# Kernel tuning notes

Measured on AMD Instinct MI355X. Metric: run time of the kernel, lower is better.

Reference implementation:

```python
import jax, jax.numpy as jnp
import numpy as np

# FTDEA(e_hidden=300, r_hidden=100, t_hidden=100)
N_NODES = 50000
N_EDGES = 250000
N_EDGES_ALL = 500000
N_REL = 300
EH, RH, TH = 300, 100, 100


def _seg_softmax(logits, seg, num):
    # torch_geometric.utils.softmax: segment-wise stable softmax
    m = jax.ops.segment_max(logits, seg, num_segments=num)
    e = jnp.exp(logits - m[seg])
    s = jax.ops.segment_sum(e, seg, num_segments=num)
    return e / s[seg]


def _gcn(x, j, i, n):
    deg = jax.ops.segment_sum(jnp.ones(i.shape[0], x.dtype), i, num_segments=n)
    dinv = jnp.where(deg > 0, 1.0 / jnp.sqrt(jnp.maximum(deg, 1.0)), 0.0)
    norm = dinv[j] * dinv[i]
    return jax.nn.relu(jax.ops.segment_sum(norm[:, None] * x[j], i, num_segments=n))


def setup_inputs():
    key = jax.random.key(0)
    ks = jax.random.split(key, 32)
    f32 = jnp.float32

    def w(k, shape):
        return jax.random.normal(k, shape, f32) / np.float32(np.sqrt(shape[0]))

    inp = {
        "x": jax.random.normal(ks[0], (N_NODES, EH), f32),
        "edge_index": jax.random.randint(ks[1], (2, N_EDGES), 0, N_NODES),
        "rel": jax.random.randint(ks[2], (N_EDGES,), 0, N_REL),
        "edge_index_all": jax.random.randint(ks[3], (2, N_EDGES_ALL), 0, N_NODES),
        "rel_size": jnp.arange(N_EDGES),
        "hw1_w": w(ks[4], (EH, EH)), "hw1_b": jnp.zeros((EH,), f32),
        "hw2_w": w(ks[5], (EH, EH)), "hw2_b": jnp.zeros((EH,), f32),
        "tc1_w": w(ks[6], (EH, TH)), "tc1_b": jnp.zeros((TH,), f32),
        "sr1_w": w(ks[7], (2 * TH, RH)), "sr1_b": jnp.zeros((RH,), f32),
        "a1_w": w(ks[8], (RH,)), "a5_w": w(ks[9], (RH,)),
        "wr_w": w(ks[10], (RH + 2 * TH, EH)), "wr_b": jnp.zeros((EH,), f32),
        "wr1_w": w(ks[11], (RH + 2 * TH, EH)), "wr1_b": jnp.zeros((EH,), f32),
        "wr2_w": w(ks[12], (RH + 2 * TH, EH)), "wr2_b": jnp.zeros((EH,), f32),
        "ah_w": w(ks[13], (EH,)), "ah1_w": w(ks[14], (EH,)), "at_w": w(ks[15], (EH,)),
        "ar1_w": w(ks[16], (EH,)), "ar2_w": w(ks[17], (EH,)), "ar3_w": w(ks[18], (EH,)),
        "ai_w": w(ks[19], (EH,)), "aj_w": w(ks[20], (EH,)),
        "fc_w": w(ks[21], (2 * EH,)), "fc_b": jnp.zeros((1,), f32),
    }
    return inp


def _forward(x, hw1_w, hw1_b, hw2_w, hw2_b, tc1_w, tc1_b, sr1_w, sr1_b, a1_w, a5_w,
             wr_w, wr_b, wr1_w, wr1_b, wr2_w, wr2_b, ah_w, ah1_w, at_w,
             ar1_w, ar2_w, ar3_w, ai_w, aj_w, fc_w, fc_b,
             edge_index, rel, edge_index_all, rel_size):
    N = x.shape[0]
    E = rel.shape[0]
    h, t = edge_index[0], edge_index[1]
    j, i = edge_index_all[0], edge_index_all[1]
    lrelu = jax.nn.leaky_relu  # slope 0.01 == F.leaky_relu default

    def highway(x1, x2, wg, bg):
        gate = jax.nn.sigmoid(x1 @ wg + bg)
        return gate * x2 + (1.0 - gate) * x1

    x = highway(x, _gcn(x, j, i, N), hw1_w, hw1_b)
    x = highway(x, _gcn(x, j, i, N), hw2_w, hw2_b)

    # --- GATt_to_R. NB: FTDEA overwrites gat_e_to_r output with zeros, so
    # x_res1 input is all-zeros and GAT_E_to_R is mathematically dead code.
    # Also r_in_t1 aliases r_in_t in the torch code, so the in-place per-relation
    # mean loop rewrites BOTH -> r_in_t1 = per-relation mean features.
    s = x @ tc1_w + tc1_b                                    # [N, t]
    cnt = jnp.maximum(jax.ops.segment_sum(jnp.ones(E, x.dtype), rel, num_segments=N_REL), 1.0)[:, None]
    mh = jax.ops.segment_sum(s[h], rel, num_segments=N_REL) / cnt
    mt = jax.ops.segment_sum(s[t], rel, num_segments=N_REL) / cnt
    r_in_t1 = jnp.concatenate([mh, mt], axis=1)[rel]         # [E, 2t]
    x_res2 = r_in_t1 @ sr1_w + sr1_b                         # [E, r]
    x_res1 = jnp.zeros((E, RH), x.dtype)                     # zeroed GAT_E_to_R output
    e1 = x_res2 @ a1_w + x_res1 @ a5_w                       # [E]
    alpha = _seg_softmax(lrelu(e1), rel, N_REL)
    x_type = jax.ops.segment_sum(alpha[:, None] * x_res2[rel_size], rel, num_segments=N_REL)  # spmm
    r_f = jnp.concatenate([x_res1 + x_type[rel], r_in_t1], axis=1)   # [E, r+2t]

    # --- GATr_to_e: three attention rounds (head, tail, head) ---
    def r2e(x_e, wr, br, a_node, a_rel, idx):
        e_r = r_f @ wr + br                                  # [E, e]
        logits = x_e[idx] @ a_node + e_r @ a_rel             # [E]
        a = _seg_softmax(lrelu(logits), idx, N)
        agg = jax.nn.relu(jax.ops.segment_sum(a[:, None] * e_r[rel_size], idx, num_segments=N))
        return x_e + agg

    x = r2e(x, wr_w, wr_b, ah_w, ar1_w, h)
    x = r2e(x, wr1_w, wr1_b, at_w, ar2_w, t)
    x = r2e(x, wr2_w, wr2_b, ah1_w, ar3_w, h)

    # --- GAT_act over edge_index_all ---
    logits = (x @ ai_w)[i] + (x @ aj_w)[j]
    a = _seg_softmax(lrelu(logits), i, N)
    g = jax.nn.relu(jax.ops.segment_sum(a[:, None] * x[j], i, num_segments=N))

    return jnp.concatenate([x, g], axis=1) @ fc_w + fc_b[0]  # [N]


def reference(x, edge_index, rel, edge_index_all, rel_size, hw1_w, hw1_b, hw2_w, hw2_b,
              tc1_w, tc1_b, sr1_w, sr1_b, a1_w, a5_w, wr_w, wr_b, wr1_w, wr1_b,
              wr2_w, wr2_b, ah_w, ah1_w, at_w, ar1_w, ar2_w, ar3_w, ai_w, aj_w, fc_w, fc_b):
    return _forward(x, hw1_w, hw1_b, hw2_w, hw2_b, tc1_w, tc1_b, sr1_w, sr1_b, a1_w, a5_w,
                    wr_w, wr_b, wr1_w, wr1_b, wr2_w, wr2_b, ah_w, ah1_w, at_w,
                    ar1_w, ar2_w, ar3_w, ai_w, aj_w, fc_w, fc_b,
                    edge_index, rel, edge_index_all, rel_size)
```

## Files before the change

kernel.cpp:

```cpp
#include <hip/hip_runtime.h>
#include <hip/hip_bf16.h>

typedef __hip_bfloat16 bf16;
typedef __attribute__((ext_vector_type(8))) short bf16x8_t;
typedef __attribute__((ext_vector_type(8))) unsigned short u16x8;
typedef __attribute__((ext_vector_type(4))) float f32x4_t;

__device__ __forceinline__ float b2f(bf16 v){ return __bfloat162float(v); }
__device__ __forceinline__ bf16 f2b(float v){ return __float2bfloat16(v); }
__device__ __forceinline__ short tobits(float v){ bf16 b = f2b(v); return *(short*)&b; }
__device__ __forceinline__ float us2f(ushort u){ return __uint_as_float(((unsigned)u)<<16); }
__device__ __forceinline__ ushort f2us(float v){ bf16 b = f2b(v); return *(ushort*)&b; }

#define NN 50000
#define NN128 50048
#define NE 250000
#define NEA 500000
#define NR 300
#define EHD 300
#define THD 100
#define RHD 100
#define XP 320
#define ERP 320
#define RCH 8
#define NBN 98
#define NBR 75

__device__ __forceinline__ int clampi(int v, int n){ return ((unsigned)v < (unsigned)n) ? v : 0; }

__device__ __forceinline__ int rdl_i(int v, int l){ return __builtin_amdgcn_readlane(v, l); }
__device__ __forceinline__ float rdl_f(float v, int l){ return __int_as_float(__builtin_amdgcn_readlane(__float_as_int(v), l)); }

typedef const __attribute__((address_space(1))) unsigned int* gas1_t;
typedef __attribute__((address_space(3))) unsigned int* las3_t;
__device__ __forceinline__ void glds16(const void* g, void* l){
    __builtin_amdgcn_global_load_lds((gas1_t)g, (las3_t)l, 16, 0, 0);
}

__device__ __forceinline__ float dpp_sum(float x){
    int v;
    v = __builtin_amdgcn_update_dpp(0, __float_as_int(x), 0x111, 0xf, 0xf, true); x += __int_as_float(v);
    v = __builtin_amdgcn_update_dpp(0, __float_as_int(x), 0x112, 0xf, 0xf, true); x += __int_as_float(v);
    v = __builtin_amdgcn_update_dpp(0, __float_as_int(x), 0x114, 0xf, 0xf, true); x += __int_as_float(v);
    v = __builtin_amdgcn_update_dpp(0, __float_as_int(x), 0x118, 0xf, 0xf, true); x += __int_as_float(v);
    v = __builtin_amdgcn_update_dpp(0, __float_as_int(x), 0x142, 0xf, 0xf, true); x += __int_as_float(v);
    v = __builtin_amdgcn_update_dpp(0, __float_as_int(x), 0x143, 0xf, 0xf, true); x += __int_as_float(v);
    return __int_as_float(__builtin_amdgcn_readlane(__float_as_int(x), 63));
}
__device__ __forceinline__ float dpp_max(float x){
    int v;
    v = __builtin_amdgcn_update_dpp(__float_as_int(x), __float_as_int(x), 0x111, 0xf, 0xf, false); x = fmaxf(x, __int_as_float(v));
    v = __builtin_amdgcn_update_dpp(__float_as_int(x), __float_as_int(x), 0x112, 0xf, 0xf, false); x = fmaxf(x, __int_as_float(v));
    v = __builtin_amdgcn_update_dpp(__float_as_int(x), __float_as_int(x), 0x114, 0xf, 0xf, false); x = fmaxf(x, __int_as_float(v));
    v = __builtin_amdgcn_update_dpp(__float_as_int(x), __float_as_int(x), 0x118, 0xf, 0xf, false); x = fmaxf(x, __int_as_float(v));
    v = __builtin_amdgcn_update_dpp(__float_as_int(x), __float_as_int(x), 0x142, 0xf, 0xf, false); x = fmaxf(x, __int_as_float(v));
    v = __builtin_amdgcn_update_dpp(__float_as_int(x), __float_as_int(x), 0x143, 0xf, 0xf, false); x = fmaxf(x, __int_as_float(v));
    return __int_as_float(__builtin_amdgcn_readlane(__float_as_int(x), 63));
}

__global__ void k_prep(const float* __restrict__ xin, ushort* __restrict__ xFu,
                       const float* __restrict__ hw1w, const float* __restrict__ hw2w,
                       const float* __restrict__ tc1w,
                       short* __restrict__ Wt1, short* __restrict__ Wt2, short* __restrict__ Wtc,
                       const float* __restrict__ ahw, const float* __restrict__ atw,
                       const float* __restrict__ ah1w, const float* __restrict__ ajw,
                       const float* __restrict__ aiw, const float* __restrict__ fcw,
                       float* __restrict__ apad, int* __restrict__ bcnt){
    int i = blockIdx.x*256 + threadIdx.x;
    if(i < 512) bcnt[i] = 0;
    const int NC = NN*40;
    const int S1 = NC + 320*320;
    const int S2 = S1 + 320*320;
    const int S3 = S2 + 128*320;
    const int S4 = S3 + 7*XP;
    if(i < NC){
        int nrow = i/40, c8 = i - nrow*40, c = c8*8;
        ushort o[8];
        if(c + 8 <= EHD){
            const float4* src = (const float4*)(xin + (size_t)nrow*EHD + c);
            float4 v0 = src[0], v1 = src[1];
            o[0]=f2us(v0.x); o[1]=f2us(v0.y); o[2]=f2us(v0.z); o[3]=f2us(v0.w);
            o[4]=f2us(v1.x); o[5]=f2us(v1.y); o[6]=f2us(v1.z); o[7]=f2us(v1.w);
        } else {
            #pragma unroll
            for(int k=0;k<8;k++){
                int cc = c + k;
                o[k] = (cc < EHD) ? f2us(xin[(size_t)nrow*EHD + cc]) : (ushort)0;
            }
        }
        u16x8 w;
        #pragma unroll
        for(int k=0;k<8;k++) w[k] = o[k];
        *(u16x8*)(xFu + (size_t)nrow*XP + c) = w;
    } else if(i < S1){
        int ii = i - NC; int n = ii/320, k = ii - n*320;
        Wt1[ii] = (n < EHD && k < EHD) ? tobits(hw1w[(size_t)k*EHD + n]) : (short)0;
    } else if(i < S2){
        int ii = i - S1; int n = ii/320, k = ii - n*320;
        Wt2[ii] = (n < EHD && k < EHD) ? tobits(hw2w[(size_t)k*EHD + n]) : (short)0;
    } else if(i < S3){
        int ii = i - S2; int n = ii/320, k = ii - n*320;
        Wtc[ii] = (n < THD && k < EHD) ? tobits(tc1w[(size_t)k*THD + n]) : (short)0;
    } else if(i < S4){
        int ii = i - S3; int v = ii/XP, c = ii - v*XP;
        float val = 0.f;
        if(c < EHD){
            const float* src = (v==0)?ahw:(v==1)?atw:(v==2)?ah1w:(v==3)?ajw:(v==4)?aiw:
                               (v==5)? fcw : (fcw + EHD);
            val = src[c];
        }
        apad[ii] = val;
    }
}

__global__ __launch_bounds__(256) void k_bincnt(const int* __restrict__ ji, const int* __restrict__ ht,
                         const int* __restrict__ rel, int* __restrict__ bcnt){
    int s = blockIdx.y;
    int n_s = (s == 0) ? NEA : NE;
    int base_e = blockIdx.x*2048;
    if(base_e >= n_s) return;
    int shift = (s < 3) ? 9 : 2;
    int tid = threadIdx.x;
    __shared__ int h[128];
    if(tid < 128) h[tid] = 0;
    __syncthreads();
    #pragma unroll
    for(int u=0;u<8;u++){
        int e = base_e + u*256 + tid;
        if(e < n_s){
            int key;
            if(s == 0) key = clampi(ji[NEA + e], NN);
            else if(s == 1) key = clampi(ht[e], NN);
            else if(s == 2) key = clampi(ht[NE + e], NN);
            else key = clampi(rel[e], NR);
            atomicAdd(&h[key >> shift], 1);
        }
    }
    __syncthreads();
    if(tid < 128 && h[tid] > 0) atomicAdd(&bcnt[s*128 + tid], h[tid]);
}

__global__ void k_bscan(const int* __restrict__ bcnt, int* __restrict__ gbase, int* __restrict__ gcur){
    __shared__ int lds[512];
    int tid = threadIdx.x;
    int v = bcnt[tid];
    lds[tid] = v; __syncthreads();
    for(int st=1; st<128; st<<=1){
        int add = ((tid & 127) >= st) ? lds[tid-st] : 0;
        __syncthreads();
        lds[tid] += add;
        __syncthreads();
    }
    int s = tid >> 7, b = tid & 127;
    int excl = lds[tid] - v;
    gbase[s*129 + b] = excl;
    gcur[s*128 + b] = excl;
    if(b == 127) gbase[s*129 + 128] = lds[tid];
}

__global__ __launch_bounds__(256) void k_bin(const int* __restrict__ ji, const int* __restrict__ ht,
                      const int* __restrict__ rel, int* __restrict__ gcur,
                      int2* __restrict__ t0, int2* __restrict__ t1,
                      int2* __restrict__ t2, int2* __restrict__ t3){
    int s = blockIdx.y;
    int n_s = (s == 0) ? NEA : NE;
    int base_e = blockIdx.x*2048;
    if(base_e >= n_s) return;
    int shift = (s < 3) ? 9 : 2;
    int tid = threadIdx.x;
    __shared__ int cnt[128], lof[128], base[128];
    __shared__ int2 buf[2048];
    if(tid < 128) cnt[tid] = 0;
    __syncthreads();
    int kk[8], pp[8], bb[8], ss[8];
    #pragma unroll
    for(int u=0;u<8;u++){
        int e = base_e + u*256 + tid;
        bb[u] = -1;
        if(e < n_s){
            int key, pay;
            if(s == 0){ key = clampi(ji[NEA + e], NN); pay = clampi(ji[e], NN); }
            else if(s == 1){ key = clampi(ht[e], NN); pay = clampi(rel[e], NR); }
            else if(s == 2){ key = clampi(ht[NE + e], NN); pay = clampi(rel[e], NR); }
            else { key = clampi(rel[e], NR); pay = e; }
            int b = key >> shift;
            kk[u] = key; pp[u] = pay; bb[u] = b;
            ss[u] = atomicAdd(&cnt[b], 1);
        }
    }
    __syncthreads();
    if(tid == 0){
        int run = 0;
        for(int b=0;b<128;b++){ lof[b] = run; run += cnt[b]; }
    }
    __syncthreads();
    #pragma unroll
    for(int u=0;u<8;u++){
        if(bb[u] >= 0){
            int pos = lof[bb[u]] + ss[u];
            buf[pos] = make_int2(kk[u], pp[u]);
        }
    }
    __syncthreads();
    if(tid < 128 && cnt[tid] > 0) base[tid] = atomicAdd(&gcur[s*128 + tid], cnt[tid]);
    __syncthreads();
    int2* tmp = (s==0) ? t0 : (s==1) ? t1 : (s==2) ? t2 : t3;
    int total = lof[127] + cnt[127];
    for(int idx=tid; idx<total; idx+=256){
        int2 kp = buf[idx];
        int b = kp.x >> shift;
        tmp[base[b] + (idx - lof[b])] = kp;
    }
}

__global__ __launch_bounds__(256) void k_place(const int* __restrict__ gbase,
                        const int2* __restrict__ t0, const int2* __restrict__ t1,
                        const int2* __restrict__ t2, const int2* __restrict__ t3,
                        int* __restrict__ off_all, int* __restrict__ off_h,
                        int* __restrict__ off_t, int* __restrict__ off_r,
                        int* __restrict__ adj_all, int* __restrict__ adj_h,
                        int* __restrict__ adj_t, int* __restrict__ adj_r,
                        float* __restrict__ dinv){
    int s = blockIdx.y, b = blockIdx.x;
    int NB = (s < 3) ? NBN : NBR;
    if(b >= NB) return;
    int W = (s < 3) ? 512 : 4;
    int len = (s < 3) ? NN : NR;
    const int2* tmp = (s==0) ? t0 : (s==1) ? t1 : (s==2) ? t2 : t3;
    int* off = (s==0) ? off_all : (s==1) ? off_h : (s==2) ? off_t : off_r;
    int* adj = (s==0) ? adj_all : (s==1) ? adj_h : (s==2) ? adj_t : adj_r;
    int node0 = b*W;
    int node1 = node0 + W; if(node1 > len) node1 = len;
    int nloc = node1 - node0;
    int wstart = gbase[s*129 + b], wend = gbase[s*129 + b + 1];
    __shared__ int hist[512];
    __shared__ int cur[512];
    __shared__ int sb[256];
    int tid = threadIdx.x;
    for(int k=tid; k<nloc; k+=256) hist[k] = 0;
    __syncthreads();
    for(int idx = wstart + tid; idx < wend; idx += 256){
        int local = tmp[idx].x - node0;
        if((unsigned)local < (unsigned)nloc) atomicAdd(&hist[local], 1);
    }
    __syncthreads();
    int v0 = (2*tid   < nloc) ? hist[2*tid]   : 0;
    int v1 = (2*tid+1 < nloc) ? hist[2*tid+1] : 0;
    int ps = v0 + v1;
    sb[tid] = ps; __syncthreads();
    for(int st=1; st<256; st<<=1){
        int add = (tid >= st) ? sb[tid-st] : 0;
        __syncthreads();
        sb[tid] += add;
        __syncthreads();
    }
    int excl = sb[tid] - ps;
    if(2*tid < nloc){
        int o = wstart + excl;
        off[node0 + 2*tid] = o;
        cur[2*tid] = o;
        if(s == 0) dinv[node0 + 2*tid] = v0 > 0 ? rsqrtf((float)v0) : 0.f;
    }
    if(2*tid+1 < nloc){
        int o = wstart + excl + v0;
        off[node0 + 2*tid+1] = o;
        cur[2*tid+1] = o;
        if(s == 0) dinv[node0 + 2*tid+1] = v1 > 0 ? rsqrtf((float)v1) : 0.f;
    }
    if(b == NB-1 && tid == 0) off[len] = gbase[s*129 + 128];
    __syncthreads();
    for(int idx = wstart + tid; idx < wend; idx += 256){
        int2 kp = tmp[idx];
        int local = kp.x - node0;
        if((unsigned)local < (unsigned)nloc){
            int slot = atomicAdd(&cur[local], 1);
            adj[slot] = kp.y;
        }
    }
}

__global__ void k_gcn(const bf16* __restrict__ xs, bf16* __restrict__ xd,
                      const int* __restrict__ off, const int* __restrict__ adjj,
                      const float* __restrict__ dinv){
    int wid = threadIdx.x >> 6, lane = threadIdx.x & 63;
    int n = blockIdx.x*4 + wid;
    if(n >= NN) return;
    float di = dinv[n];
    int s0 = off[n], s1 = off[n+1], cnt = s1 - s0;
    bool act = lane < 40;
    float c0=0,c1=0,c2=0,c3=0,c4=0,c5=0,c6=0,c7=0;
    if(cnt > 0 && cnt <= 64){
        int jl = (lane < cnt) ? clampi(adjj[s0+lane], NN) : 0;
        float dl = (lane < cnt) ? dinv[jl] : 0.f;
        int it = 0;
        for(; it+4 <= cnt; it += 4){
            int j0=rdl_i(jl,it), j1=rdl_i(jl,it+1), j2=rdl_i(jl,it+2), j3=rdl_i(jl,it+3);
            float n0=di*rdl_f(dl,it), n1=di*rdl_f(dl,it+1), n2=di*rdl_f(dl,it+2), n3=di*rdl_f(dl,it+3);
            if(act){
                u16x8 v0 = ((const u16x8*)(xs + (size_t)j0*XP))[lane];
                u16x8 v1 = ((const u16x8*)(xs + (size_t)j1*XP))[lane];
                u16x8 v2 = ((const u16x8*)(xs + (size_t)j2*XP))[lane];
                u16x8 v3 = ((const u16x8*)(xs + (size_t)j3*XP))[lane];
                c0 += n0*us2f(v0[0])+n1*us2f(v1[0])+n2*us2f(v2[0])+n3*us2f(v3[0]);
                c1 += n0*us2f(v0[1])+n1*us2f(v1[1])+n2*us2f(v2[1])+n3*us2f(v3[1]);
                c2 += n0*us2f(v0[2])+n1*us2f(v1[2])+n2*us2f(v2[2])+n3*us2f(v3[2]);
                c3 += n0*us2f(v0[3])+n1*us2f(v1[3])+n2*us2f(v2[3])+n3*us2f(v3[3]);
                c4 += n0*us2f(v0[4])+n1*us2f(v1[4])+n2*us2f(v2[4])+n3*us2f(v3[4]);
                c5 += n0*us2f(v0[5])+n1*us2f(v1[5])+n2*us2f(v2[5])+n3*us2f(v3[5]);
                c6 += n0*us2f(v0[6])+n1*us2f(v1[6])+n2*us2f(v2[6])+n3*us2f(v3[6]);
                c7 += n0*us2f(v0[7])+n1*us2f(v1[7])+n2*us2f(v2[7])+n3*us2f(v3[7]);
            }
        }
        for(; it < cnt; it++){
            int j0 = rdl_i(jl, it);
            float n0 = di*rdl_f(dl, it);
            if(act){
                u16x8 v0 = ((const u16x8*)(xs + (size_t)j0*XP))[lane];
                c0 += n0*us2f(v0[0]); c1 += n0*us2f(v0[1]); c2 += n0*us2f(v0[2]); c3 += n0*us2f(v0[3]);
                c4 += n0*us2f(v0[4]); c5 += n0*us2f(v0[5]); c6 += n0*us2f(v0[6]); c7 += n0*us2f(v0[7]);
            }
        }
    } else if(cnt > 64){
        for(int it=s0; it<s1; it++){
            int j = clampi(adjj[it], NN);
            float nr = di * dinv[j];
            if(act){
                u16x8 v0 = ((const u16x8*)(xs + (size_t)j*XP))[lane];
                c0 += nr*us2f(v0[0]); c1 += nr*us2f(v0[1]); c2 += nr*us2f(v0[2]); c3 += nr*us2f(v0[3]);
                c4 += nr*us2f(v0[4]); c5 += nr*us2f(v0[5]); c6 += nr*us2f(v0[6]); c7 += nr*us2f(v0[7]);
            }
        }
    }
    if(act){
        u16x8 w;
        w[0]=f2us(fmaxf(c0,0.f)); w[1]=f2us(fmaxf(c1,0.f)); w[2]=f2us(fmaxf(c2,0.f)); w[3]=f2us(fmaxf(c3,0.f));
        w[4]=f2us(fmaxf(c4,0.f)); w[5]=f2us(fmaxf(c5,0.f)); w[6]=f2us(fmaxf(c6,0.f)); w[7]=f2us(fmaxf(c7,0.f));
        ((u16x8*)(xd + (size_t)n*XP))[lane] = w;
    }
}

template<int MODE>
__global__ __launch_bounds__(256) void k_gemm_mfma(const bf16* __restrict__ X,
                       const short* __restrict__ Wt, const float* __restrict__ bias,
                       bf16* __restrict__ out, const bf16* __restrict__ Xprev,
                       int M, int K, int Ncols, int ldOut){
    __shared__ short As[64*32];
    __shared__ short Bs[64*32];
    int tid = threadIdx.x;
    int bm = blockIdx.x*64, bn = blockIdx.y*64;
    int wid = tid>>6, lane = tid&63;
    int wm = (wid&1)*32, wn = (wid>>1)*32;
    int lm = lane&15, lq = lane>>4;
    f32x4_t acc00={0,0,0,0}, acc01={0,0,0,0}, acc10={0,0,0,0}, acc11={0,0,0,0};
    int srow = tid>>2, ssl = tid&3;
    int ssl_sw = ssl ^ ((srow>>1)&3);
    short* ldsA = As + (size_t)(wid*64)*8;
    short* ldsB = Bs + (size_t)(wid*64)*8;
    const bf16*  gA = X  + (size_t)(bm + srow)*K + ssl_sw*8;
    const short* gB = Wt + (size_t)(bn + srow)*K + ssl_sw*8;
    for(int k0=0; k0<K; k0+=32){
        glds16(gA + k0, ldsA);
        glds16(gB + k0, ldsB);
        __syncthreads();
        int ra0 = wm + lm, ra1 = wm + 16 + lm;
        int rb0 = wn + lm, rb1 = wn + 16 + lm;
        bf16x8_t a0 = *(const bf16x8_t*)(As + ra0*32 + ((lq ^ ((ra0>>1)&3))*8));
        bf16x8_t a1 = *(const bf16x8_t*)(As + ra1*32 + ((lq ^ ((ra1>>1)&3))*8));
        bf16x8_t b0 = *(const bf16x8_t*)(Bs + rb0*32 + ((lq ^ ((rb0>>1)&3))*8));
        bf16x8_t b1 = *(const bf16x8_t*)(Bs + rb1*32 + ((lq ^ ((rb1>>1)&3))*8));
        acc00 = __builtin_amdgcn_mfma_f32_16x16x32_bf16(a0, b0, acc00, 0, 0, 0);
        acc01 = __builtin_amdgcn_mfma_f32_16x16x32_bf16(a0, b1, acc01, 0, 0, 0);
        acc10 = __builtin_amdgcn_mfma_f32_16x16x32_bf16(a1, b0, acc10, 0, 0, 0);
        acc11 = __builtin_amdgcn_mfma_f32_16x16x32_bf16(a1, b1, acc11, 0, 0, 0);
        __syncthreads();
    }
    #pragma unroll
    for(int tm=0;tm<2;tm++){
        #pragma unroll
        for(int tn=0;tn<2;tn++){
            f32x4_t a = tm==0 ? (tn==0 ? acc00 : acc01) : (tn==0 ? acc10 : acc11);
            int gn = bn + wn + tn*16 + lm;
            if(gn >= Ncols) continue;
            float bi = bias[gn];
            #pragma unroll
            for(int r=0;r<4;r++){
                int gm = bm + wm + tm*16 + lq*4 + r;
                if(gm >= M) continue;
                float t = a[r] + bi;
                size_t p = (size_t)gm*ldOut + gn;
                if(MODE == 0){
                    out[p] = f2b(t);
                } else {
                    float g = __builtin_amdgcn_rcpf(1.f + __expf(-t));
                    out[p] = f2b(g*b2f(out[p]) + (1.f - g)*b2f(Xprev[p]));
                }
            }
        }
    }
}

__global__ void k_relsum2(const bf16* __restrict__ s, const int* __restrict__ ht,
                          const int* __restrict__ off_r, const int* __restrict__ adj_r,
                          float* __restrict__ RFpart){
    int r = blockIdx.x, c = blockIdx.y, d = threadIdx.x;
    if(d >= THD) return;
    int s0 = off_r[r], s1 = off_r[r+1];
    int cnt = s1 - s0;
    float ah = 0.f, at2 = 0.f;
    if(cnt > 0){
        int per = (cnt + RCH - 1)/RCH;
        int lo = s0 + c*per, hi = lo + per; if(hi > s1) hi = s1;
        for(int it=lo; it<hi; it++){
            int e = clampi(adj_r[it], NE);
            int hh = clampi(ht[e], NN), tt = clampi(ht[NE + e], NN);
            ah  += b2f(s[(size_t)hh*THD + d]);
            at2 += b2f(s[(size_t)tt*THD + d]);
        }
    }
    size_t base = (size_t)(r*RCH + c)*2*THD;
    RFpart[base + d] = ah;
    RFpart[base + THD + d] = at2;
}

__global__ void k_relfin(const float* __restrict__ sr1w, const float* __restrict__ sr1b,
                         const int* __restrict__ off_r, const float* __restrict__ RFpart,
                         float* __restrict__ RF){
    int r = blockIdx.x, d = threadIdx.x;
    int cnt = off_r[r+1] - off_r[r];
    float inv = 1.f/(float)(cnt > 1 ? cnt : 1);
    if(d < THD){
        float a = 0.f, b = 0.f;
        #pragma unroll
        for(int c=0;c<RCH;c++){
            size_t base = (size_t)(r*RCH + c)*2*THD;
            a += RFpart[base + d];
            b += RFpart[base + THD + d];
        }
        RF[(size_t)r*EHD + THD   + d] = a*inv;
        RF[(size_t)r*EHD + 2*THD + d] = b*inv;
    }
    __syncthreads();
    if(d < RHD){
        float v = 0.f;
        if(cnt > 0){
            v = sr1b[d];
            for(int k2=0; k2<2*THD; k2++) v += RF[(size_t)r*EHD + THD + k2] * sr1w[k2*RHD + d];
        }
        RF[(size_t)r*EHD + d] = v;
    }
}

__global__ void k_reler(const float* __restrict__ RF,
                        const float* w0, const float* b0, const float* w1, const float* b1,
                        const float* w2, const float* b2,
                        const float* ar1, const float* ar2, const float* ar3,
                        float* __restrict__ ER, float* __restrict__ cvec){
    int r = blockIdx.x, kk = blockIdx.y;
    const float* w = kk==0 ? w0 : (kk==1 ? w1 : w2);
    const float* b = kk==0 ? b0 : (kk==1 ? b1 : b2);
    const float* a = kk==0 ? ar1 : (kk==1 ? ar2 : ar3);
    int tid = threadIdx.x;
    __shared__ float rfs[EHD];
    for(int d=tid; d<EHD; d+=256) rfs[d] = RF[(size_t)r*EHD + d];
    __syncthreads();
    float pd = 0.f;
    for(int o = tid; o < ERP; o += 256){
        float v = 0.f;
        if(o < EHD){
            v = b[o];
            for(int d=0; d<EHD; d++) v += rfs[d] * w[(size_t)d*EHD + o];
            pd += v * a[o];
        }
        ER[((size_t)kk*NR + r)*ERP + o] = v;
    }
    __shared__ float red[4];
    pd = dpp_sum(pd);
    if((tid & 63) == 0) red[tid>>6] = pd;
    __syncthreads();
    if(tid == 0) cvec[kk*NR + r] = red[0]+red[1]+red[2]+red[3];
}

__device__ __forceinline__ void r2e_round(float* xv, bool act, int lane, int s0, int s1,
        int rl, float cval,
        const int* __restrict__ adjrel, const float* __restrict__ ERk,
        const float* __restrict__ ck, const float* __restrict__ an){
    float p = 0.f;
    if(act){
        const float4* a4 = (const float4*)an;
        float4 a0 = a4[2*lane], a1 = a4[2*lane+1];
        p = xv[0]*a0.x + xv[1]*a0.y + xv[2]*a0.z + xv[3]*a0.w
          + xv[4]*a1.x + xv[5]*a1.y + xv[6]*a1.z + xv[7]*a1.w;
    }
    p = dpp_sum(p);
    int cnt = s1 - s0;
    if(cnt <= 0) return;
    float c0=0,c1=0,c2=0,c3=0,c4=0,c5=0,c6=0,c7=0;
    if(cnt <= 64){
        float lg = p + cval;
        lg = lg > 0 ? lg : 0.01f*lg;
        float mx = dpp_max((lane < cnt) ? lg : -1e30f);
        float ex = (lane < cnt) ? __expf(lg - mx) : 0.f;
        float al = ex * __builtin_amdgcn_rcpf(dpp_sum(ex));
        int it = 0;
        for(; it+2 <= cnt; it += 2){
            int r0i = rdl_i(rl, it), r1i = rdl_i(rl, it+1);
            float q0 = rdl_f(al, it), q1 = rdl_f(al, it+1);
            if(act){
                const float4* e0p = (const float4*)(ERk + (size_t)r0i*ERP);
                const float4* e1p = (const float4*)(ERk + (size_t)r1i*ERP);
                float4 e0 = e0p[2*lane], e1 = e1p[2*lane];
                float4 f0 = e0p[2*lane+1], f1 = e1p[2*lane+1];
                c0 += q0*e0.x + q1*e1.x; c1 += q0*e0.y + q1*e1.y;
                c2 += q0*e0.z + q1*e1.z; c3 += q0*e0.w + q1*e1.w;
                c4 += q0*f0.x + q1*f1.x; c5 += q0*f0.y + q1*f1.y;
                c6 += q0*f0.z + q1*f1.z; c7 += q0*f0.w + q1*f1.w;
            }
        }
        if(it < cnt){
            int r0i = rdl_i(rl, it);
            float q0 = rdl_f(al, it);
            if(act){
                const float4* e0p = (const float4*)(ERk + (size_t)r0i*ERP);
                float4 e0 = e0p[2*lane], f0 = e0p[2*lane+1];
                c0 += q0*e0.x; c1 += q0*e0.y; c2 += q0*e0.z; c3 += q0*e0.w;
                c4 += q0*f0.x; c5 += q0*f0.y; c6 += q0*f0.z; c7 += q0*f0.w;
            }
        }
    } else {
        float mx = -1e30f;
        for(int it=s0; it<s1; it++){
            float lg = p + ck[clampi(adjrel[it], NR)];
            lg = lg > 0 ? lg : 0.01f*lg;
            mx = fmaxf(mx, lg);
        }
        float ssum = 0.f;
        for(int it=s0; it<s1; it++){
            float lg = p + ck[clampi(adjrel[it], NR)];
            lg = lg > 0 ? lg : 0.01f*lg;
            ssum += __expf(lg - mx);
        }
        float rinv = __builtin_amdgcn_rcpf(ssum);
        for(int it=s0; it<s1; it++){
            int r = clampi(adjrel[it], NR);
            float lg = p + ck[r];
            lg = lg > 0 ? lg : 0.01f*lg;
            float aw = __expf(lg - mx)*rinv;
            if(act){
                const float4* er4 = (const float4*)(ERk + (size_t)r*ERP);
                float4 e0 = er4[2*lane], f0 = er4[2*lane+1];
                c0 += aw*e0.x; c1 += aw*e0.y; c2 += aw*e0.z; c3 += aw*e0.w;
                c4 += aw*f0.x; c5 += aw*f0.y; c6 += aw*f0.z; c7 += aw*f0.w;
            }
        }
    }
    xv[0] += fmaxf(c0,0.f); xv[1] += fmaxf(c1,0.f); xv[2] += fmaxf(c2,0.f); xv[3] += fmaxf(c3,0.f);
    xv[4] += fmaxf(c4,0.f); xv[5] += fmaxf(c5,0.f); xv[6] += fmaxf(c6,0.f); xv[7] += fmaxf(c7,0.f);
}

__global__ void k_r2e3(bf16* __restrict__ x,
                       const int* __restrict__ off_h, const int* __restrict__ adj_h,
                       const int* __restrict__ off_t, const int* __restrict__ adj_t,
                       const float* __restrict__ ER, const float* __restrict__ cvec,
                       const float* __restrict__ apad, float* __restrict__ ajv){
    int wid = threadIdx.x >> 6, lane = threadIdx.x & 63;
    int n = blockIdx.x*4 + wid;
    if(n >= NN) return;
    bool act = lane < 40;
    u16x8* xr = (u16x8*)(x + (size_t)n*XP);
    float xv[8];
    if(act){
        u16x8 v = xr[lane];
        #pragma unroll
        for(int k=0;k<8;k++) xv[k] = us2f(v[k]);
    } else {
        #pragma unroll
        for(int k=0;k<8;k++) xv[k] = 0.f;
    }
    int h0 = off_h[n], h1 = off_h[n+1];
    int t0_ = off_t[n], t1_ = off_t[n+1];
    int hcnt = h1 - h0, tcnt = t1_ - t0_;
    int rlh = (hcnt > 0 && hcnt <= 64 && lane < hcnt) ? clampi(adj_h[h0+lane], NR) : 0;
    int rlt = (tcnt > 0 && tcnt <= 64 && lane < tcnt) ? clampi(adj_t[t0_+lane], NR) : 0;
    float ch1 = cvec[rlh], ctv = cvec[NR + rlt], ch3 = cvec[2*NR + rlh];
    r2e_round(xv, act, lane, h0, h1, rlh, ch1, adj_h, ER,                    cvec,      apad);
    r2e_round(xv, act, lane, t0_, t1_, rlt, ctv, adj_t, ER + (size_t)NR*ERP, cvec+NR,   apad + XP);
    r2e_round(xv, act, lane, h0, h1, rlh, ch3, adj_h, ER + (size_t)2*NR*ERP, cvec+2*NR, apad + 2*XP);
    {
        float p = 0.f;
        if(act){
            const float4* a4 = (const float4*)(apad + 3*XP);
            float4 a0 = a4[2*lane], a1 = a4[2*lane+1];
            p = xv[0]*a0.x + xv[1]*a0.y + xv[2]*a0.z + xv[3]*a0.w
              + xv[4]*a1.x + xv[5]*a1.y + xv[6]*a1.z + xv[7]*a1.w;
        }
        p = dpp_sum(p);
        if(lane == 0) ajv[n] = p;
    }
    if(act){
        u16x8 w;
        #pragma unroll
        for(int k=0;k<8;k++) w[k] = f2us(xv[k]);
        xr[lane] = w;
    }
}

__global__ void k_final(const bf16* __restrict__ x, const float* __restrict__ ajv,
                        const int* __restrict__ off, const int* __restrict__ adjj,
                        const float* __restrict__ apad, const float* __restrict__ fcb,
                        float* __restrict__ out){
    int wid = threadIdx.x >> 6, lane = threadIdx.x & 63;
    int n = blockIdx.x*4 + wid;
    if(n >= NN) return;
    bool act = lane < 40;
    float xv[8];
    if(act){
        u16x8 v = ((const u16x8*)(x + (size_t)n*XP))[lane];
        #pragma unroll
        for(int k=0;k<8;k++) xv[k] = us2f(v[k]);
    } else {
        #pragma unroll
        for(int k=0;k<8;k++) xv[k] = 0.f;
    }
    float p = 0.f;
    if(act){
        const float4* a4 = (const float4*)(apad + 4*XP);
        float4 a0 = a4[2*lane], a1 = a4[2*lane+1];
        p = xv[0]*a0.x + xv[1]*a0.y + xv[2]*a0.z + xv[3]*a0.w
          + xv[4]*a1.x + xv[5]*a1.y + xv[6]*a1.z + xv[7]*a1.w;
    }
    p = dpp_sum(p);
    int s0 = off[n], s1 = off[n+1], cnt = s1 - s0;
    float c0=0,c1=0,c2=0,c3=0,c4=0,c5=0,c6=0,c7=0;
    if(cnt > 0 && cnt <= 64){
        int jl = (lane < cnt) ? clampi(adjj[s0+lane], NN) : 0;
        float av = (lane < cnt) ? ajv[jl] : 0.f;
        float lg = p + av;
        lg = lg > 0 ? lg : 0.01f*lg;
        float mx = dpp_max((lane < cnt) ? lg : -1e30f);
        float ex = (lane < cnt) ? __expf(lg - mx) : 0.f;
        float al = ex * __builtin_amdgcn_rcpf(dpp_sum(ex));
        int it = 0;
        for(; it+4 <= cnt; it += 4){
            int j0=rdl_i(jl,it), j1=rdl_i(jl,it+1), j2=rdl_i(jl,it+2), j3=rdl_i(jl,it+3);
            float q0=rdl_f(al,it), q1=rdl_f(al,it+1), q2=rdl_f(al,it+2), q3=rdl_f(al,it+3);
            if(act){
                u16x8 v0 = ((const u16x8*)(x + (size_t)j0*XP))[lane];
                u16x8 v1 = ((const u16x8*)(x + (size_t)j1*XP))[lane];
                u16x8 v2 = ((const u16x8*)(x + (size_t)j2*XP))[lane];
                u16x8 v3 = ((const u16x8*)(x + (size_t)j3*XP))[lane];
                c0 += q0*us2f(v0[0])+q1*us2f(v1[0])+q2*us2f(v2[0])+q3*us2f(v3[0]);
                c1 += q0*us2f(v0[1])+q1*us2f(v1[1])+q2*us2f(v2[1])+q3*us2f(v3[1]);
                c2 += q0*us2f(v0[2])+q1*us2f(v1[2])+q2*us2f(v2[2])+q3*us2f(v3[2]);
                c3 += q0*us2f(v0[3])+q1*us2f(v1[3])+q2*us2f(v2[3])+q3*us2f(v3[3]);
                c4 += q0*us2f(v0[4])+q1*us2f(v1[4])+q2*us2f(v2[4])+q3*us2f(v3[4]);
                c5 += q0*us2f(v0[5])+q1*us2f(v1[5])+q2*us2f(v2[5])+q3*us2f(v3[5]);
                c6 += q0*us2f(v0[6])+q1*us2f(v1[6])+q2*us2f(v2[6])+q3*us2f(v3[6]);
                c7 += q0*us2f(v0[7])+q1*us2f(v1[7])+q2*us2f(v2[7])+q3*us2f(v3[7]);
            }
        }
        for(; it < cnt; it++){
            int j0 = rdl_i(jl, it);
            float q0 = rdl_f(al, it);
            if(act){
                u16x8 v0 = ((const u16x8*)(x + (size_t)j0*XP))[lane];
                c0 += q0*us2f(v0[0]); c1 += q0*us2f(v0[1]); c2 += q0*us2f(v0[2]); c3 += q0*us2f(v0[3]);
                c4 += q0*us2f(v0[4]); c5 += q0*us2f(v0[5]); c6 += q0*us2f(v0[6]); c7 += q0*us2f(v0[7]);
            }
        }
    } else if(cnt > 64){
        float mx = -1e30f;
        for(int it=s0; it<s1; it++){
            float lg = p + ajv[clampi(adjj[it], NN)];
            lg = lg > 0 ? lg : 0.01f*lg;
            mx = fmaxf(mx, lg);
        }
        float ssum = 0.f;
        for(int it=s0; it<s1; it++){
            float lg = p + ajv[clampi(adjj[it], NN)];
            lg = lg > 0 ? lg : 0.01f*lg;
            ssum += __expf(lg - mx);
        }
        float rinv = __builtin_amdgcn_rcpf(ssum);
        for(int it=s0; it<s1; it++){
            int j = clampi(adjj[it], NN);
            float lg = p + ajv[j];
            lg = lg > 0 ? lg : 0.01f*lg;
            float aw = __expf(lg - mx)*rinv;
            if(act){
                u16x8 v0 = ((const u16x8*)(x + (size_t)j*XP))[lane];
                c0 += aw*us2f(v0[0]); c1 += aw*us2f(v0[1]); c2 += aw*us2f(v0[2]); c3 += aw*us2f(v0[3]);
                c4 += aw*us2f(v0[4]); c5 += aw*us2f(v0[5]); c6 += aw*us2f(v0[6]); c7 += aw*us2f(v0[7]);
            }
        }
    }
    float part = 0.f;
    if(act){
        const float4* f5 = (const float4*)(apad + 5*XP);
        const float4* f6 = (const float4*)(apad + 6*XP);
        float4 u0 = f5[2*lane], u1 = f5[2*lane+1];
        float4 g0 = f6[2*lane], g1 = f6[2*lane+1];
        part = xv[0]*u0.x + xv[1]*u0.y + xv[2]*u0.z + xv[3]*u0.w
             + xv[4]*u1.x + xv[5]*u1.y + xv[6]*u1.z + xv[7]*u1.w
             + fmaxf(c0,0.f)*g0.x + fmaxf(c1,0.f)*g0.y + fmaxf(c2,0.f)*g0.z + fmaxf(c3,0.f)*g0.w
             + fmaxf(c4,0.f)*g1.x + fmaxf(c5,0.f)*g1.y + fmaxf(c6,0.f)*g1.z + fmaxf(c7,0.f)*g1.w;
    }
    part = dpp_sum(part);
    if(lane == 0) out[n] = part + fcb[0];
}

extern "C" void kernel_launch(void* const* d_in, const int* in_sizes, int n_in,
                              void* d_out, int out_size, void* d_ws, size_t ws_size,
                              hipStream_t stream){
    const float* x_in = (const float*)d_in[0];
    const int*  ht   = (const int*)d_in[1];
    const int*  rel  = (const int*)d_in[2];
    const int*  ji   = (const int*)d_in[3];
    const float* hw1w=(const float*)d_in[5];  const float* hw1b=(const float*)d_in[6];
    const float* hw2w=(const float*)d_in[7];  const float* hw2b=(const float*)d_in[8];
    const float* tc1w=(const float*)d_in[9];  const float* tc1b=(const float*)d_in[10];
    const float* sr1w=(const float*)d_in[11]; const float* sr1b=(const float*)d_in[12];
    const float* wrw =(const float*)d_in[15]; const float* wrb =(const float*)d_in[16];
    const float* wr1w=(const float*)d_in[17]; const float* wr1b=(const float*)d_in[18];
    const float* wr2w=(const float*)d_in[19]; const float* wr2b=(const float*)d_in[20];
    const float* ahw =(const float*)d_in[21]; const float* ah1w=(const float*)d_in[22];
    const float* atw =(const float*)d_in[23];
    const float* ar1 =(const float*)d_in[24]; const float* ar2 =(const float*)d_in[25];
    const float* ar3 =(const float*)d_in[26];
    const float* aiw =(const float*)d_in[27]; const float* ajw =(const float*)d_in[28];
    const float* fcw =(const float*)d_in[29]; const float* fcb =(const float*)d_in[30];
    float* out = (float*)d_out;

    char* w = (char*)d_ws;
    auto alloc = [&](size_t bytes)->char*{ char* p = w; w += (bytes + 255)/256*256; return p; };
    bf16* xF = (bf16*)alloc((size_t)NN128*XP*2);
    bf16* B  = (bf16*)alloc((size_t)NN128*XP*2);
    char* Bc = (char*)B;
    int2* tmp_all = (int2*)(Bc);
    int2* tmp_h   = (int2*)(Bc + 4u*1024*1024);
    int2* tmp_t   = (int2*)(Bc + 8u*1024*1024);
    int2* tmp_r   = (int2*)(Bc + 12u*1024*1024);
    bf16*  sbuf   = (bf16*)(Bc);
    float* RF     = (float*)(Bc + 11u*1024*1024);
    float* RFpart = (float*)(Bc + 12u*1024*1024);
    float* ER     = (float*)(Bc + 14u*1024*1024);
    float* cvec   = (float*)(Bc + 15u*1024*1024 + 512u*1024);
    float* ajv    = (float*)(Bc + 16u*1024*1024);
    short* Wt1 = (short*)alloc((size_t)320*320*2);
    short* Wt2 = (short*)alloc((size_t)320*320*2);
    short* Wtc = (short*)alloc((size_t)128*320*2);
    float* apad = (float*)alloc((size_t)7*XP*4);
    float* dinv = (float*)alloc((size_t)NN*4);
    int* off_all=(int*)alloc((NN+1)*4);
    int* adj_all=(int*)alloc((size_t)NEA*4);
    int* off_h  =(int*)alloc((NN+1)*4);
    int* adj_h  =(int*)alloc((size_t)NE*4);
    int* off_t  =(int*)alloc((NN+1)*4);
    int* adj_t  =(int*)alloc((size_t)NE*4);
    int* off_r  =(int*)alloc((NR+1)*4);
    int* adj_r  =(int*)alloc((size_t)NE*4);
    int* bcnt   =(int*)alloc(512*4);
    int* gbase  =(int*)alloc(4*129*4);
    int* gcur   =(int*)alloc(4*128*4);

    const int PRT = NN*40 + 2*320*320 + 128*320 + 7*XP;
    k_prep<<<dim3((PRT+255)/256), dim3(256), 0, stream>>>(x_in, (ushort*)xF, hw1w, hw2w, tc1w,
                                                          Wt1, Wt2, Wtc,
                                                          ahw, atw, ah1w, ajw, aiw, fcw,
                                                          apad, bcnt);
    k_bincnt<<<dim3((NEA+2047)/2048, 4), dim3(256), 0, stream>>>(ji, ht, rel, bcnt);
    k_bscan<<<dim3(1), dim3(512), 0, stream>>>(bcnt, gbase, gcur);
    k_bin<<<dim3((NEA+2047)/2048, 4), dim3(256), 0, stream>>>(ji, ht, rel, gcur,
                                                              tmp_all, tmp_h, tmp_t, tmp_r);
    k_place<<<dim3(NBN, 4), dim3(256), 0, stream>>>(gbase, tmp_all, tmp_h, tmp_t, tmp_r,
                                                    off_all, off_h, off_t, off_r,
                                                    adj_all, adj_h, adj_t, adj_r, dinv);

    const int nb4 = (NN+3)/4;
    const dim3 gg((NN128)/64, (EHD+63)/64);
    k_gcn<<<dim3(nb4), dim3(256), 0, stream>>>(xF, B, off_all, adj_all, dinv);
    k_gemm_mfma<1><<<gg, dim3(256), 0, stream>>>(xF, Wt1, hw1b, B, xF, NN, XP, EHD, XP);
    k_gcn<<<dim3(nb4), dim3(256), 0, stream>>>(B, xF, off_all, adj_all, dinv);
    k_gemm_mfma<1><<<gg, dim3(256), 0, stream>>>(B, Wt2, hw2b, xF, B, NN, XP, EHD, XP);
    k_gemm_mfma<0><<<dim3(NN128/64, (THD+63)/64), dim3(256), 0, stream>>>(xF, Wtc, tc1b, sbuf, xF, NN, XP, THD, THD);
    k_relsum2<<<dim3(NR, RCH), dim3(128), 0, stream>>>(sbuf, ht, off_r, adj_r, RFpart);
    k_relfin<<<dim3(NR), dim3(128), 0, stream>>>(sr1w, sr1b, off_r, RFpart, RF);
    k_reler<<<dim3(NR, 3), dim3(256), 0, stream>>>(RF, wrw, wrb, wr1w, wr1b, wr2w, wr2b,
                                                   ar1, ar2, ar3, ER, cvec);
    k_r2e3<<<dim3(nb4), dim3(256), 0, stream>>>(xF, off_h, adj_h, off_t, adj_t, ER, cvec,
                                                apad, ajv);
    k_final<<<dim3(nb4), dim3(256), 0, stream>>>(xF, ajv, off_all, adj_all, apad, fcb, out);
}
```

Measured before the change: 629.8 us.

## Fuse prep with bin counting, fold relfin into reler, XCD-aware GEMM tile mapping

Merges the edge-bin counting into the prep kernel as extra blocks and zeroes the counters with a memset, removing one launch. The relation-feature finalize kernel is folded into k_reler, so each block recomputes the per-relation mean and sr1 projection itself. This duplicates that work three times (one per kk) but drops a kernel and the RF round trip. GEMM launches become 1D grids remapped so consecutive logical tiles land on the same XCD, for better L2 reuse of the A panel.

```diff
diff --git a/kernel.cpp b/kernel.cpp
--- a/kernel.cpp
+++ b/kernel.cpp
@@ -25,6 +25,8 @@
 #define RCH 8
 #define NBN 98
 #define NBR 75
+#define PREP_NB 8782
+#define BCNT_NB 245
 
 __device__ __forceinline__ int clampi(int v, int n){ return ((unsigned)v < (unsigned)n) ? v : 0; }
 
@@ -58,16 +60,44 @@
     return __int_as_float(__builtin_amdgcn_readlane(__float_as_int(x), 63));
 }
 
-__global__ void k_prep(const float* __restrict__ xin, ushort* __restrict__ xFu,
+__global__ __launch_bounds__(256) void k_prepc(const float* __restrict__ xin, ushort* __restrict__ xFu,
                        const float* __restrict__ hw1w, const float* __restrict__ hw2w,
                        const float* __restrict__ tc1w,
                        short* __restrict__ Wt1, short* __restrict__ Wt2, short* __restrict__ Wtc,
                        const float* __restrict__ ahw, const float* __restrict__ atw,
                        const float* __restrict__ ah1w, const float* __restrict__ ajw,
                        const float* __restrict__ aiw, const float* __restrict__ fcw,
-                       float* __restrict__ apad, int* __restrict__ bcnt){
-    int i = blockIdx.x*256 + threadIdx.x;
-    if(i < 512) bcnt[i] = 0;
+                       float* __restrict__ apad, int* __restrict__ bcnt,
+                       const int* __restrict__ ji, const int* __restrict__ ht,
+                       const int* __restrict__ rel){
+    int blk = blockIdx.x, tid = threadIdx.x;
+    __shared__ int h[128];
+    if(blk >= PREP_NB){
+        int eb = blk - PREP_NB;
+        int s = eb/BCNT_NB, bx = eb - s*BCNT_NB;
+        int n_s = (s == 0) ? NEA : NE;
+        int base_e = bx*2048;
+        if(base_e >= n_s) return;
+        int shift = (s < 3) ? 9 : 2;
+        if(tid < 128) h[tid] = 0;
+        __syncthreads();
+        #pragma unroll
+        for(int u=0;u<8;u++){
+            int e = base_e + u*256 + tid;
+            if(e < n_s){
+                int key;
+                if(s == 0) key = clampi(ji[NEA + e], NN);
+                else if(s == 1) key = clampi(ht[e], NN);
+                else if(s == 2) key = clampi(ht[NE + e], NN);
+                else key = clampi(rel[e], NR);
+                atomicAdd(&h[key >> shift], 1);
+            }
+        }
+        __syncthreads();
+        if(tid < 128 && h[tid] > 0) atomicAdd(&bcnt[s*128 + tid], h[tid]);
+        return;
+    }
+    int i = blk*256 + tid;
     const int NC = NN*40;
     const int S1 = NC + 320*320;
     const int S2 = S1 + 320*320;
@@ -111,33 +141,6 @@
         }
         apad[ii] = val;
     }
-}
-
-__global__ __launch_bounds__(256) void k_bincnt(const int* __restrict__ ji, const int* __restrict__ ht,
-                         const int* __restrict__ rel, int* __restrict__ bcnt){
-    int s = blockIdx.y;
-    int n_s = (s == 0) ? NEA : NE;
-    int base_e = blockIdx.x*2048;
-    if(base_e >= n_s) return;
-    int shift = (s < 3) ? 9 : 2;
-    int tid = threadIdx.x;
-    __shared__ int h[128];
-    if(tid < 128) h[tid] = 0;
-    __syncthreads();
-    #pragma unroll
-    for(int u=0;u<8;u++){
-        int e = base_e + u*256 + tid;
-        if(e < n_s){
-            int key;
-            if(s == 0) key = clampi(ji[NEA + e], NN);
-            else if(s == 1) key = clampi(ht[e], NN);
-            else if(s == 2) key = clampi(ht[NE + e], NN);
-            else key = clampi(rel[e], NR);
-            atomicAdd(&h[key >> shift], 1);
-        }
-    }
-    __syncthreads();
-    if(tid < 128 && h[tid] > 0) atomicAdd(&bcnt[s*128 + tid], h[tid]);
 }
 
 __global__ void k_bscan(const int* __restrict__ bcnt, int* __restrict__ gbase, int* __restrict__ gcur){
@@ -343,11 +346,17 @@
 __global__ __launch_bounds__(256) void k_gemm_mfma(const bf16* __restrict__ X,
                        const short* __restrict__ Wt, const float* __restrict__ bias,
                        bf16* __restrict__ out, const bf16* __restrict__ Xprev,
-                       int M, int K, int Ncols, int ldOut){
+                       int M, int K, int Ncols, int ldOut, int ncb){
     __shared__ short As[64*32];
     __shared__ short Bs[64*32];
     int tid = threadIdx.x;
-    int bm = blockIdx.x*64, bn = blockIdx.y*64;
+    int bid = blockIdx.x;
+    int nwg = gridDim.x;
+    int xcd = bid & 7, idx = bid >> 3;
+    int q = nwg >> 3, rr = nwg & 7;
+    int logical = (xcd < rr ? xcd*(q+1) : rr*(q+1) + (xcd-rr)*q) + idx;
+    int pan = logical / ncb;
+    int bm = pan*64, bn = (logical - pan*ncb)*64;
     int wid = tid>>6, lane = tid&63;
     int wm = (wid&1)*32, wn = (wid>>1)*32;
     int lm = lane&15, lq = lane>>4;
@@ -422,35 +431,8 @@
     RFpart[base + THD + d] = at2;
 }
 
-__global__ void k_relfin(const float* __restrict__ sr1w, const float* __restrict__ sr1b,
-                         const int* __restrict__ off_r, const float* __restrict__ RFpart,
-                         float* __restrict__ RF){
-    int r = blockIdx.x, d = threadIdx.x;
-    int cnt = off_r[r+1] - off_r[r];
-    float inv = 1.f/(float)(cnt > 1 ? cnt : 1);
-    if(d < THD){
-        float a = 0.f, b = 0.f;
-        #pragma unroll
-        for(int c=0;c<RCH;c++){
-            size_t base = (size_t)(r*RCH + c)*2*THD;
-            a += RFpart[base + d];
-            b += RFpart[base + THD + d];
-        }
-        RF[(size_t)r*EHD + THD   + d] = a*inv;
-        RF[(size_t)r*EHD + 2*THD + d] = b*inv;
-    }
-    __syncthreads();
-    if(d < RHD){
-        float v = 0.f;
-        if(cnt > 0){
-            v = sr1b[d];
-            for(int k2=0; k2<2*THD; k2++) v += RF[(size_t)r*EHD + THD + k2] * sr1w[k2*RHD + d];
-        }
-        RF[(size_t)r*EHD + d] = v;
-    }
-}
-
-__global__ void k_reler(const float* __restrict__ RF,
+__global__ void k_reler(const float* __restrict__ RFpart, const int* __restrict__ off_r,
+                        const float* __restrict__ sr1w, const float* __restrict__ sr1b,
                         const float* w0, const float* b0, const float* w1, const float* b1,
                         const float* w2, const float* b2,
                         const float* ar1, const float* ar2, const float* ar3,
@@ -461,7 +443,23 @@
     const float* a = kk==0 ? ar1 : (kk==1 ? ar2 : ar3);
     int tid = threadIdx.x;
     __shared__ float rfs[EHD];
-    for(int d=tid; d<EHD; d+=256) rfs[d] = RF[(size_t)r*EHD + d];
+    int cnt = off_r[r+1] - off_r[r];
+    float inv = 1.f/(float)(cnt > 1 ? cnt : 1);
+    for(int d=tid; d<2*THD; d+=256){
+        float sacc = 0.f;
+        #pragma unroll
+        for(int c=0;c<RCH;c++) sacc += RFpart[(size_t)(r*RCH + c)*2*THD + d];
+        rfs[THD + d] = sacc*inv;
+    }
+    __syncthreads();
+    if(tid < RHD){
+        float v = 0.f;
+        if(cnt > 0){
+            v = sr1b[tid];
+            for(int k2=0; k2<2*THD; k2++) v += rfs[THD + k2] * sr1w[k2*RHD + tid];
+        }
+        rfs[tid] = v;
+    }
     __syncthreads();
     float pd = 0.f;
     for(int o = tid; o < ERP; o += 256){
@@ -740,7 +738,6 @@
     int2* tmp_t   = (int2*)(Bc + 8u*1024*1024);
     int2* tmp_r   = (int2*)(Bc + 12u*1024*1024);
     bf16*  sbuf   = (bf16*)(Bc);
-    float* RF     = (float*)(Bc + 11u*1024*1024);
     float* RFpart = (float*)(Bc + 12u*1024*1024);
     float* ER     = (float*)(Bc + 14u*1024*1024);
     float* cvec   = (float*)(Bc + 15u*1024*1024 + 512u*1024);
@@ -762,12 +759,11 @@
     int* gbase  =(int*)alloc(4*129*4);
     int* gcur   =(int*)alloc(4*128*4);
 
-    const int PRT = NN*40 + 2*320*320 + 128*320 + 7*XP;
-    k_prep<<<dim3((PRT+255)/256), dim3(256), 0, stream>>>(x_in, (ushort*)xF, hw1w, hw2w, tc1w,
+    hipMemsetAsync(bcnt, 0, 512*4, stream);
+    k_prepc<<<dim3(PREP_NB + 4*BCNT_NB), dim3(256), 0, stream>>>(x_in, (ushort*)xF, hw1w, hw2w, tc1w,
                                                           Wt1, Wt2, Wtc,
                                                           ahw, atw, ah1w, ajw, aiw, fcw,
-                                                          apad, bcnt);
-    k_bincnt<<<dim3((NEA+2047)/2048, 4), dim3(256), 0, stream>>>(ji, ht, rel, bcnt);
+                                                          apad, bcnt, ji, ht, rel);
     k_bscan<<<dim3(1), dim3(512), 0, stream>>>(bcnt, gbase, gcur);
     k_bin<<<dim3((NEA+2047)/2048, 4), dim3(256), 0, stream>>>(ji, ht, rel, gcur,
                                                               tmp_all, tmp_h, tmp_t, tmp_r);
@@ -776,15 +772,14 @@
                                                     adj_all, adj_h, adj_t, adj_r, dinv);
 
     const int nb4 = (NN+3)/4;
-    const dim3 gg((NN128)/64, (EHD+63)/64);
     k_gcn<<<dim3(nb4), dim3(256), 0, stream>>>(xF, B, off_all, adj_all, dinv);
-    k_gemm_mfma<1><<<gg, dim3(256), 0, stream>>>(xF, Wt1, hw1b, B, xF, NN, XP, EHD, XP);
+    k_gemm_mfma<1><<<dim3((NN128/64)*5), dim3(256), 0, stream>>>(xF, Wt1, hw1b, B, xF, NN, XP, EHD, XP, 5);
     k_gcn<<<dim3(nb4), dim3(256), 0, stream>>>(B, xF, off_all, adj_all, dinv);
-    k_gemm_mfma<1><<<gg, dim3(256), 0, stream>>>(B, Wt2, hw2b, xF, B, NN, XP, EHD, XP);
-    k_gemm_mfma<0><<<dim3(NN128/64, (THD+63)/64), dim3(256), 0, stream>>>(xF, Wtc, tc1b, sbuf, xF, NN, XP, THD, THD);
+    k_gemm_mfma<1><<<dim3((NN128/64)*5), dim3(256), 0, stream>>>(B, Wt2, hw2b, xF, B, NN, XP, EHD, XP, 5);
+    k_gemm_mfma<0><<<dim3((NN128/64)*2), dim3(256), 0, stream>>>(xF, Wtc, tc1b, sbuf, xF, NN, XP, THD, THD, 2);
     k_relsum2<<<dim3(NR, RCH), dim3(128), 0, stream>>>(sbuf, ht, off_r, adj_r, RFpart);
-    k_relfin<<<dim3(NR), dim3(128), 0, stream>>>(sr1w, sr1b, off_r, RFpart, RF);
-    k_reler<<<dim3(NR, 3), dim3(256), 0, stream>>>(RF, wrw, wrb, wr1w, wr1b, wr2w, wr2b,
+    k_reler<<<dim3(NR, 3), dim3(256), 0, stream>>>(RFpart, off_r, sr1w, sr1b,
+                                                   wrw, wrb, wr1w, wr1b, wr2w, wr2b,
                                                    ar1, ar2, ar3, ER, cvec);
     k_r2e3<<<dim3(nb4), dim3(256), 0, stream>>>(xF, off_h, adj_h, off_t, adj_t, ER, cvec,
                                                 apad, ajv);
```

After: 610.7 us. 1.03x faster.
